# Kernel tuning notes

Measured on AMD Instinct MI355X. Metric: run time of the kernel, lower is better.

## Reference

```python
import jax, jax.numpy as jnp
import numpy as np

NUM_HIGH = 3
CHANNELS = 3

def _gauss_kernel(channels):
    k = jnp.array([[1., 4., 6., 4., 1.],
                   [4., 16., 24., 16., 4.],
                   [6., 24., 36., 24., 6.],
                   [4., 16., 24., 16., 4.],
                   [1., 4., 6., 4., 1.]], dtype=jnp.float32) / 256.0
    # depthwise kernel layout OIHW with I=1, O=channels
    return jnp.broadcast_to(k, (channels, 1, 5, 5))

def conv_gauss(img, kernel):
    # reflect-pad by 2 on H,W then depthwise (grouped) 5x5 conv, VALID
    p = jnp.pad(img, ((0, 0), (0, 0), (2, 2), (2, 2)), mode='reflect')
    return jax.lax.conv_general_dilated(
        p, kernel, window_strides=(1, 1), padding='VALID',
        feature_group_count=img.shape[1],
        dimension_numbers=('NCHW', 'OIHW', 'NCHW'))

def downsample(x):
    return x[:, :, ::2, ::2]

def upsample(x, kernel):
    B, C, H, W = x.shape
    x_up = jnp.zeros((B, C, 2 * H, 2 * W), dtype=x.dtype).at[:, :, ::2, ::2].set(x)
    return conv_gauss(x_up, 4.0 * kernel)

def setup_inputs() -> dict:
    key = jax.random.key(0)
    img = jax.random.normal(key, (8, CHANNELS, 1024, 1024), dtype=jnp.float32)
    kernel = _gauss_kernel(CHANNELS)
    return {"img": img, "kernel": kernel}

def reference(img, kernel):
    # pyramid_decom: Laplacian pyramid (H,W divisible by 2**NUM_HIGH, so no interpolate)
    current = img
    pyr = []
    for _ in range(NUM_HIGH):
        filtered = conv_gauss(current, kernel)
        down = downsample(filtered)
        up = upsample(down, kernel)
        pyr.append(current - up)
        current = down
    pyr.append(current)
    return tuple(pyr)
```

## Files before the change

kernel.cpp:

```cpp
#include <hip/hip_runtime.h>

#define TILE 64
#define SCW 72
#define SCP 76
#define SDW 34
#define SDP 36

__device__ __forceinline__ int refl(int t, int n) {
    if (t < 0) t = -t;
    if (t >= n) t = 2 * (n - 1) - t;
    return t;
}

__global__ __launch_bounds__(256) void lap_level_kernel(
    const float* __restrict__ cur, float* __restrict__ lap,
    float* __restrict__ down, int H, int W)
{
    __shared__ float s_cur[SCW][SCP];
    __shared__ float s_down[SDW][SDP];

    const int x0 = blockIdx.x * TILE, y0 = blockIdx.y * TILE;
    const int img = blockIdx.z;
    const int Hh = H >> 1, Wh = W >> 1;
    const int tid = threadIdx.x;
    const int tx = tid & 15, ty = tid >> 4;

    const float* curb = cur + (size_t)img * H * W;

    const bool border = (x0 == 0) | (y0 == 0) | (x0 + TILE == W) | (y0 + TILE == H);
    if (!border) {
        const float* src = curb + (size_t)(y0 - 4) * W + (x0 - 4);
        for (int k = tid; k < SCW * 18; k += 256) {
            unsigned r = (unsigned)k / 18u;
            unsigned c4 = (unsigned)k - r * 18u;
            *(float4*)&s_cur[r][c4 * 4] =
                *(const float4*)(src + (size_t)r * W + c4 * 4);
        }
    } else {
        for (int k = tid; k < SCW * SCW; k += 256) {
            unsigned r = (unsigned)k / 72u;
            unsigned c = (unsigned)k - r * 72u;
            s_cur[r][c] = curb[(size_t)refl(y0 - 4 + (int)r, H) * W
                               + refl(x0 - 4 + (int)c, W)];
        }
    }
    __syncthreads();

    const int dy0 = (y0 >> 1) - 1, dx0 = (x0 >> 1) - 1;
    float* downb = down + (size_t)img * Hh * Wh;
    for (int k = tid; k < SDW * SDW; k += 256) {
        unsigned dy = (unsigned)k / 34u;
        unsigned dx = (unsigned)k - dy * 34u;
        const int rb = 2 * (int)dy, cb = 2 * (int)dx;
        float acc = 0.f;
        const float wr[5] = {1.f, 4.f, 6.f, 4.f, 1.f};
#pragma unroll
        for (int u = 0; u < 5; ++u) {
            const float* row = &s_cur[rb + u][cb];
            float2 p0 = *(const float2*)(row);
            float2 p1 = *(const float2*)(row + 2);
            float2 p2 = *(const float2*)(row + 4);
            float rs = p0.x + 4.f * p0.y + 6.f * p1.x + 4.f * p1.y + p2.x;
            acc += wr[u] * rs;
        }
        acc *= (1.0f / 256.0f);
        s_down[dy][dx] = acc;
        if (dy - 1u < 32u && dx - 1u < 32u)
            downb[(size_t)(dy0 + (int)dy) * Wh + (dx0 + (int)dx)] = acc;
    }
    __syncthreads();

    float d[4][4];
#pragma unroll
    for (int r = 0; r < 4; ++r) {
        float2 a = *(const float2*)&s_down[2 * ty + r][2 * tx];
        float2 b = *(const float2*)&s_down[2 * ty + r][2 * tx + 2];
        d[r][0] = a.x; d[r][1] = a.y; d[r][2] = b.x; d[r][3] = b.y;
    }
    float ve[2][4], vo[2][4];
#pragma unroll
    for (int r2 = 0; r2 < 2; ++r2)
#pragma unroll
        for (int c = 0; c < 4; ++c) {
            ve[r2][c] = d[r2][c] + 6.f * d[r2 + 1][c] + d[r2 + 2][c];
            vo[r2][c] = 4.f * (d[r2 + 1][c] + d[r2 + 2][c]);
        }

    float* lapb = lap + (size_t)img * H * W;
    const int ib = y0 + 4 * ty, jb = x0 + 4 * tx;
#pragma unroll
    for (int rr = 0; rr < 4; ++rr) {
        const int r2 = rr >> 1;
        float4 cv = *(const float4*)&s_cur[4 * ty + 4 + rr][4 * tx + 4];
        float u0, u1, u2, u3;
        if ((rr & 1) == 0) {
            u0 = ve[r2][0] + 6.f * ve[r2][1] + ve[r2][2];
            u1 = 4.f * (ve[r2][1] + ve[r2][2]);
            u2 = ve[r2][1] + 6.f * ve[r2][2] + ve[r2][3];
            u3 = 4.f * (ve[r2][2] + ve[r2][3]);
        } else {
            u0 = vo[r2][0] + 6.f * vo[r2][1] + vo[r2][2];
            u1 = 4.f * (vo[r2][1] + vo[r2][2]);
            u2 = vo[r2][1] + 6.f * vo[r2][2] + vo[r2][3];
            u3 = 4.f * (vo[r2][2] + vo[r2][3]);
        }
        float4 o;
        o.x = cv.x - u0 * (1.f / 64.f);
        o.y = cv.y - u1 * (1.f / 64.f);
        o.z = cv.z - u2 * (1.f / 64.f);
        o.w = cv.w - u3 * (1.f / 64.f);
        *(float4*)(lapb + (size_t)(ib + rr) * W + jb) = o;
    }
}

extern "C" void kernel_launch(void* const* d_in, const int* in_sizes, int n_in,
                              void* d_out, int out_size, void* d_ws, size_t ws_size,
                              hipStream_t stream) {
    const float* img = (const float*)d_in[0];
    float* out = (float*)d_out;

    const long long BC = 8LL * 3;
    const long long n0 = BC * 1024 * 1024;
    const long long n1 = BC * 512 * 512;
    const long long n2 = BC * 256 * 256;

    float* out0 = out;
    float* out1 = out0 + n0;
    float* out2 = out1 + n1;
    float* out3 = out2 + n2;

    float* ws0 = (float*)d_ws;
    float* ws1 = ws0 + n1;

    lap_level_kernel<<<dim3(1024 / TILE, 1024 / TILE, (int)BC), 256, 0, stream>>>(
        img, out0, ws0, 1024, 1024);
    lap_level_kernel<<<dim3(512 / TILE, 512 / TILE, (int)BC), 256, 0, stream>>>(
        ws0, out1, ws1, 512, 512);
    lap_level_kernel<<<dim3(256 / TILE, 256 / TILE, (int)BC), 256, 0, stream>>>(
        ws1, out2, out3, 256, 256);
}
```

Before: 86.77 us.

## Fuse first two pyramid levels into one kernel with enlarged halo tile

Adds a kernel that computes levels 0 and 1 in a single pass. Each block loads an 83x83 halo tile, builds the level-1 downsample and the level-2 downsample in shared memory, and writes both Laplacian outputs plus the quarter-resolution image. This removes one launch and the global write and reread of the level-1 intermediate. In exchange it recomputes overlapping halos, uses more shared memory per block, and needs reflect-index handling at the second level.

```diff
diff --git a/kernel.cpp b/kernel.cpp
--- a/kernel.cpp
+++ b/kernel.cpp
@@ -1,16 +1,183 @@
 #include <hip/hip_runtime.h>
 
 #define TILE 64
-#define SCW 72
-#define SCP 76
-#define SDW 34
-#define SDP 36
 
 __device__ __forceinline__ int refl(int t, int n) {
     if (t < 0) t = -t;
     if (t >= n) t = 2 * (n - 1) - t;
     return t;
 }
+
+#define SC_H 83
+#define SC_W 84
+#define D0_N 39
+#define D0_P 40
+#define D1_N 18
+#define D1_P 20
+
+__global__ __launch_bounds__(256) void lap2level_kernel(
+    const float* __restrict__ cur, float* __restrict__ lap0,
+    float* __restrict__ lap1, float* __restrict__ down1,
+    int H, int W)
+{
+    __shared__ float s_cur[SC_H][SC_W];
+    __shared__ float s_d0[D0_N][D0_P];
+    __shared__ float s_d1[D1_N][D1_P];
+
+    const int x0 = blockIdx.x * TILE, y0 = blockIdx.y * TILE;
+    const int img = blockIdx.z;
+    const int Hh = H >> 1, Wh = W >> 1, Wq = W >> 2;
+    const int tid = threadIdx.x;
+    const int tx = tid & 15, ty = tid >> 4;
+
+    const float* curb = cur + (size_t)img * H * W;
+
+    const bool border = (x0 == 0) | (y0 == 0) | (x0 + TILE == W) | (y0 + TILE == H);
+    if (!border) {
+        const float* src = curb + (size_t)(y0 - 12) * W + (x0 - 12);
+        for (int k = tid; k < SC_H * 21; k += 256) {
+            unsigned r = (unsigned)k / 21u;
+            unsigned c4 = (unsigned)k - r * 21u;
+            *(float4*)&s_cur[r][c4 * 4] = *(const float4*)(src + (size_t)r * W + c4 * 4);
+        }
+    } else {
+        for (int k = tid; k < SC_H * SC_H; k += 256) {
+            unsigned r = (unsigned)k / 83u;
+            unsigned c = (unsigned)k - r * 83u;
+            s_cur[r][c] = curb[(size_t)refl(y0 - 12 + (int)r, H) * W
+                               + refl(x0 - 12 + (int)c, W)];
+        }
+    }
+    __syncthreads();
+
+    for (int k = tid; k < D0_N * D0_N; k += 256) {
+        unsigned a = (unsigned)k / 39u;
+        unsigned b = (unsigned)k - a * 39u;
+        const int rb = 2 * (int)a + 2, cb = 2 * (int)b + 2;
+        const float wv[5] = {1.f, 4.f, 6.f, 4.f, 1.f};
+        float acc = 0.f;
+#pragma unroll
+        for (int u = 0; u < 5; ++u) {
+            const float* row = &s_cur[rb + u][cb];
+            float2 p0 = *(const float2*)row;
+            float2 p1 = *(const float2*)(row + 2);
+            float rs = p0.x + 4.f * p0.y + 6.f * p1.x + 4.f * p1.y + row[4];
+            acc += wv[u] * rs;
+        }
+        s_d0[a][b] = acc * (1.0f / 256.0f);
+    }
+    __syncthreads();
+
+    const int dy0f = (y0 >> 1) - 4, dx0f = (x0 >> 1) - 4;
+    for (int k = tid; k < D1_N * D1_N; k += 256) {
+        unsigned e = (unsigned)k / 18u;
+        unsigned f = (unsigned)k - e * 18u;
+        int ar[5], bc[5];
+#pragma unroll
+        for (int u = 0; u < 5; ++u) {
+            int dyt = dy0f + 2 * (int)e + u;
+            int ov = dyt - (Hh - 1); if (ov < 0) ov = 0;
+            ar[u] = 2 * (int)e + u - 2 * ov;
+            int dxt = dx0f + 2 * (int)f + u;
+            int ow = dxt - (Wh - 1); if (ow < 0) ow = 0;
+            bc[u] = 2 * (int)f + u - 2 * ow;
+        }
+        const float wv[5] = {1.f, 4.f, 6.f, 4.f, 1.f};
+        float acc = 0.f;
+#pragma unroll
+        for (int u = 0; u < 5; ++u) {
+            float rs = 0.f;
+#pragma unroll
+            for (int v = 0; v < 5; ++v) rs += wv[v] * s_d0[ar[u]][bc[v]];
+            acc += wv[u] * rs;
+        }
+        s_d1[e][f] = acc * (1.0f / 256.0f);
+    }
+    __syncthreads();
+
+    {
+        float* d1b = down1 + (size_t)img * (Hh >> 1) * Wq;
+        int e = (tid >> 4) + 1, f = (tid & 15) + 1;
+        d1b[(size_t)((y0 >> 2) + e - 1) * Wq + ((x0 >> 2) + f - 1)] = s_d1[e][f];
+    }
+
+    {
+        float d[4][4];
+#pragma unroll
+        for (int r = 0; r < 4; ++r)
+#pragma unroll
+            for (int c = 0; c < 4; ++c)
+                d[r][c] = s_d0[2 * ty + 3 + r][2 * tx + 3 + c];
+        float ve[2][4], vo[2][4];
+#pragma unroll
+        for (int r2 = 0; r2 < 2; ++r2)
+#pragma unroll
+            for (int c = 0; c < 4; ++c) {
+                ve[r2][c] = d[r2][c] + 6.f * d[r2 + 1][c] + d[r2 + 2][c];
+                vo[r2][c] = 4.f * (d[r2 + 1][c] + d[r2 + 2][c]);
+            }
+        float* lap0b = lap0 + (size_t)img * H * W;
+        const int ib = y0 + 4 * ty, jb = x0 + 4 * tx;
+#pragma unroll
+        for (int rr = 0; rr < 4; ++rr) {
+            const int r2 = rr >> 1;
+            float4 cv = *(const float4*)&s_cur[4 * ty + 12 + rr][4 * tx + 12];
+            float u0, u1, u2, u3;
+            if ((rr & 1) == 0) {
+                u0 = ve[r2][0] + 6.f * ve[r2][1] + ve[r2][2];
+                u1 = 4.f * (ve[r2][1] + ve[r2][2]);
+                u2 = ve[r2][1] + 6.f * ve[r2][2] + ve[r2][3];
+                u3 = 4.f * (ve[r2][2] + ve[r2][3]);
+            } else {
+                u0 = vo[r2][0] + 6.f * vo[r2][1] + vo[r2][2];
+                u1 = 4.f * (vo[r2][1] + vo[r2][2]);
+                u2 = vo[r2][1] + 6.f * vo[r2][2] + vo[r2][3];
+                u3 = 4.f * (vo[r2][2] + vo[r2][3]);
+            }
+            float4 o;
+            o.x = cv.x - u0 * (1.f / 64.f);
+            o.y = cv.y - u1 * (1.f / 64.f);
+            o.z = cv.z - u2 * (1.f / 64.f);
+            o.w = cv.w - u3 * (1.f / 64.f);
+            *(float4*)(lap0b + (size_t)(ib + rr) * W + jb) = o;
+        }
+    }
+
+    {
+        float m[3][3];
+#pragma unroll
+        for (int a = 0; a < 3; ++a)
+#pragma unroll
+            for (int b = 0; b < 3; ++b)
+                m[a][b] = s_d1[ty + a][tx + b];
+        float ce[3], co[3];
+#pragma unroll
+        for (int c = 0; c < 3; ++c) {
+            ce[c] = m[0][c] + 6.f * m[1][c] + m[2][c];
+            co[c] = 4.f * (m[1][c] + m[2][c]);
+        }
+        float u00 = ce[0] + 6.f * ce[1] + ce[2];
+        float u01 = 4.f * (ce[1] + ce[2]);
+        float u10 = co[0] + 6.f * co[1] + co[2];
+        float u11 = 4.f * (co[1] + co[2]);
+        float2 c0 = *(const float2*)&s_d0[2 * ty + 4][2 * tx + 4];
+        float2 c1 = *(const float2*)&s_d0[2 * ty + 5][2 * tx + 4];
+        float* lap1b = lap1 + (size_t)img * Hh * Wh;
+        const int p0 = (y0 >> 1) + 2 * ty, q0 = (x0 >> 1) + 2 * tx;
+        float2 o0, o1;
+        o0.x = c0.x - u00 * (1.f / 64.f);
+        o0.y = c0.y - u01 * (1.f / 64.f);
+        o1.x = c1.x - u10 * (1.f / 64.f);
+        o1.y = c1.y - u11 * (1.f / 64.f);
+        *(float2*)(lap1b + (size_t)p0 * Wh + q0) = o0;
+        *(float2*)(lap1b + (size_t)(p0 + 1) * Wh + q0) = o1;
+    }
+}
+
+#define SCW 72
+#define SCP 76
+#define SDW 34
+#define SDP 36
 
 __global__ __launch_bounds__(256) void lap_level_kernel(
     const float* __restrict__ cur, float* __restrict__ lap,
@@ -33,8 +200,7 @@
         for (int k = tid; k < SCW * 18; k += 256) {
             unsigned r = (unsigned)k / 18u;
             unsigned c4 = (unsigned)k - r * 18u;
-            *(float4*)&s_cur[r][c4 * 4] =
-                *(const float4*)(src + (size_t)r * W + c4 * 4);
+            *(float4*)&s_cur[r][c4 * 4] = *(const float4*)(src + (size_t)r * W + c4 * 4);
         }
     } else {
         for (int k = tid; k < SCW * SCW; k += 256) {
@@ -52,16 +218,15 @@
         unsigned dy = (unsigned)k / 34u;
         unsigned dx = (unsigned)k - dy * 34u;
         const int rb = 2 * (int)dy, cb = 2 * (int)dx;
+        const float wv[5] = {1.f, 4.f, 6.f, 4.f, 1.f};
         float acc = 0.f;
-        const float wr[5] = {1.f, 4.f, 6.f, 4.f, 1.f};
 #pragma unroll
         for (int u = 0; u < 5; ++u) {
             const float* row = &s_cur[rb + u][cb];
             float2 p0 = *(const float2*)(row);
             float2 p1 = *(const float2*)(row + 2);
-            float2 p2 = *(const float2*)(row + 4);
-            float rs = p0.x + 4.f * p0.y + 6.f * p1.x + 4.f * p1.y + p2.x;
-            acc += wr[u] * rs;
+            float rs = p0.x + 4.f * p0.y + 6.f * p1.x + 4.f * p1.y + row[4];
+            acc += wv[u] * rs;
         }
         acc *= (1.0f / 256.0f);
         s_down[dy][dx] = acc;
@@ -130,12 +295,9 @@
     float* out3 = out2 + n2;
 
     float* ws0 = (float*)d_ws;
-    float* ws1 = ws0 + n1;
-
-    lap_level_kernel<<<dim3(1024 / TILE, 1024 / TILE, (int)BC), 256, 0, stream>>>(
-        img, out0, ws0, 1024, 1024);
-    lap_level_kernel<<<dim3(512 / TILE, 512 / TILE, (int)BC), 256, 0, stream>>>(
-        ws0, out1, ws1, 512, 512);
+
+    lap2level_kernel<<<dim3(16, 16, (int)BC), 256, 0, stream>>>(
+        img, out0, out1, ws0, 1024, 1024);
     lap_level_kernel<<<dim3(256 / TILE, 256 / TILE, (int)BC), 256, 0, stream>>>(
-        ws1, out2, out3, 256, 256);
+        ws0, out2, out3, 256, 256);
 }
```

After: 86.48 us. Within noise of the previous version (-0.3%).

## Separate the downsample blur into vertical and horizontal passes, use 512-thread blocks

Applied to the files above, without the earlier changes.

The 5x5 blur that produces the downsampled tile is split into a vertical pass, which writes into a new shared scratch buffer, and a horizontal pass that reads from it. This cuts the multiply-adds per output. The block grows to 512 threads, so each thread now produces two output rows instead of four, and the launch bound requests 8 blocks per CU. The cost is an extra barrier, about 10 KB more shared memory per block, and padding changes that may alter bank-conflict behaviour.

```diff
diff --git a/kernel.cpp b/kernel.cpp
--- a/kernel.cpp
+++ b/kernel.cpp
@@ -1,10 +1,9 @@
 #include <hip/hip_runtime.h>
 
 #define TILE 64
-#define SCW 72
 #define SCP 76
-#define SDW 34
-#define SDP 36
+#define TMP 77
+#define SDP 35
 
 __device__ __forceinline__ int refl(int t, int n) {
     if (t < 0) t = -t;
@@ -12,32 +11,31 @@
     return t;
 }
 
-__global__ __launch_bounds__(256) void lap_level_kernel(
+__global__ __launch_bounds__(512, 8) void lap_level_kernel(
     const float* __restrict__ cur, float* __restrict__ lap,
     float* __restrict__ down, int H, int W)
 {
-    __shared__ float s_cur[SCW][SCP];
-    __shared__ float s_down[SDW][SDP];
+    __shared__ float s_cur[72][SCP];
+    __shared__ float s_tmp[34][TMP];
+    __shared__ float s_down[34][SDP];
 
     const int x0 = blockIdx.x * TILE, y0 = blockIdx.y * TILE;
     const int img = blockIdx.z;
     const int Hh = H >> 1, Wh = W >> 1;
     const int tid = threadIdx.x;
-    const int tx = tid & 15, ty = tid >> 4;
 
     const float* curb = cur + (size_t)img * H * W;
 
     const bool border = (x0 == 0) | (y0 == 0) | (x0 + TILE == W) | (y0 + TILE == H);
     if (!border) {
         const float* src = curb + (size_t)(y0 - 4) * W + (x0 - 4);
-        for (int k = tid; k < SCW * 18; k += 256) {
+        for (int k = tid; k < 72 * 18; k += 512) {
             unsigned r = (unsigned)k / 18u;
-            unsigned c4 = (unsigned)k - r * 18u;
-            *(float4*)&s_cur[r][c4 * 4] =
-                *(const float4*)(src + (size_t)r * W + c4 * 4);
+            unsigned c4 = ((unsigned)k - r * 18u) * 4u;
+            *(float4*)&s_cur[r][c4] = *(const float4*)(src + (size_t)r * W + c4);
         }
     } else {
-        for (int k = tid; k < SCW * SCW; k += 256) {
+        for (int k = tid; k < 72 * 72; k += 512) {
             unsigned r = (unsigned)k / 72u;
             unsigned c = (unsigned)k - r * 72u;
             s_cur[r][c] = curb[(size_t)refl(y0 - 4 + (int)r, H) * W
@@ -46,71 +44,63 @@
     }
     __syncthreads();
 
-    const int dy0 = (y0 >> 1) - 1, dx0 = (x0 >> 1) - 1;
-    float* downb = down + (size_t)img * Hh * Wh;
-    for (int k = tid; k < SDW * SDW; k += 256) {
-        unsigned dy = (unsigned)k / 34u;
-        unsigned dx = (unsigned)k - dy * 34u;
-        const int rb = 2 * (int)dy, cb = 2 * (int)dx;
-        float acc = 0.f;
-        const float wr[5] = {1.f, 4.f, 6.f, 4.f, 1.f};
-#pragma unroll
-        for (int u = 0; u < 5; ++u) {
-            const float* row = &s_cur[rb + u][cb];
-            float2 p0 = *(const float2*)(row);
-            float2 p1 = *(const float2*)(row + 2);
-            float2 p2 = *(const float2*)(row + 4);
-            float rs = p0.x + 4.f * p0.y + 6.f * p1.x + 4.f * p1.y + p2.x;
-            acc += wr[u] * rs;
-        }
-        acc *= (1.0f / 256.0f);
-        s_down[dy][dx] = acc;
-        if (dy - 1u < 32u && dx - 1u < 32u)
-            downb[(size_t)(dy0 + (int)dy) * Wh + (dx0 + (int)dx)] = acc;
+    for (int k = tid; k < 34 * 18; k += 512) {
+        unsigned a = (unsigned)k / 18u;
+        unsigned c4 = ((unsigned)k - a * 18u) * 4u;
+        float4 r0 = *(const float4*)&s_cur[2 * a + 0][c4];
+        float4 r1 = *(const float4*)&s_cur[2 * a + 1][c4];
+        float4 r2 = *(const float4*)&s_cur[2 * a + 2][c4];
+        float4 r3 = *(const float4*)&s_cur[2 * a + 3][c4];
+        float4 r4 = *(const float4*)&s_cur[2 * a + 4][c4];
+        s_tmp[a][c4 + 0] = r0.x + 4.f * r1.x + 6.f * r2.x + 4.f * r3.x + r4.x;
+        s_tmp[a][c4 + 1] = r0.y + 4.f * r1.y + 6.f * r2.y + 4.f * r3.y + r4.y;
+        s_tmp[a][c4 + 2] = r0.z + 4.f * r1.z + 6.f * r2.z + 4.f * r3.z + r4.z;
+        s_tmp[a][c4 + 3] = r0.w + 4.f * r1.w + 6.f * r2.w + 4.f * r3.w + r4.w;
     }
     __syncthreads();
 
-    float d[4][4];
+    float* downb = down + (size_t)img * Hh * Wh;
+    for (int k = tid; k < 34 * 34; k += 512) {
+        unsigned a = (unsigned)k / 34u;
+        unsigned b = (unsigned)k - a * 34u;
+        const float* t = &s_tmp[a][2 * b];
+        float v = (t[0] + 4.f * t[1] + 6.f * t[2] + 4.f * t[3] + t[4]) * (1.f / 256.f);
+        s_down[a][b] = v;
+        if (a - 1u < 32u && b - 1u < 32u)
+            downb[(size_t)((y0 >> 1) + (int)a - 1) * Wh + ((x0 >> 1) + (int)b - 1)] = v;
+    }
+    __syncthreads();
+
+    const int tx = tid & 15, ty = tid >> 4;
+    float d0[4], d1[4], d2[4];
 #pragma unroll
-    for (int r = 0; r < 4; ++r) {
-        float2 a = *(const float2*)&s_down[2 * ty + r][2 * tx];
-        float2 b = *(const float2*)&s_down[2 * ty + r][2 * tx + 2];
-        d[r][0] = a.x; d[r][1] = a.y; d[r][2] = b.x; d[r][3] = b.y;
+    for (int c = 0; c < 4; ++c) {
+        d0[c] = s_down[ty + 0][2 * tx + c];
+        d1[c] = s_down[ty + 1][2 * tx + c];
+        d2[c] = s_down[ty + 2][2 * tx + c];
     }
-    float ve[2][4], vo[2][4];
+    float ce[4], co[4];
 #pragma unroll
-    for (int r2 = 0; r2 < 2; ++r2)
-#pragma unroll
-        for (int c = 0; c < 4; ++c) {
-            ve[r2][c] = d[r2][c] + 6.f * d[r2 + 1][c] + d[r2 + 2][c];
-            vo[r2][c] = 4.f * (d[r2 + 1][c] + d[r2 + 2][c]);
-        }
+    for (int c = 0; c < 4; ++c) {
+        ce[c] = d0[c] + 6.f * d1[c] + d2[c];
+        co[c] = 4.f * (d1[c] + d2[c]);
+    }
+    float4 cve = *(const float4*)&s_cur[4 + 2 * ty][4 + 4 * tx];
+    float4 cvo = *(const float4*)&s_cur[5 + 2 * ty][4 + 4 * tx];
+    float4 oe, oo;
+    oe.x = cve.x - (ce[0] + 6.f * ce[1] + ce[2]) * (1.f / 64.f);
+    oe.y = cve.y - 4.f * (ce[1] + ce[2]) * (1.f / 64.f);
+    oe.z = cve.z - (ce[1] + 6.f * ce[2] + ce[3]) * (1.f / 64.f);
+    oe.w = cve.w - 4.f * (ce[2] + ce[3]) * (1.f / 64.f);
+    oo.x = cvo.x - (co[0] + 6.f * co[1] + co[2]) * (1.f / 64.f);
+    oo.y = cvo.y - 4.f * (co[1] + co[2]) * (1.f / 64.f);
+    oo.z = cvo.z - (co[1] + 6.f * co[2] + co[3]) * (1.f / 64.f);
+    oo.w = cvo.w - 4.f * (co[2] + co[3]) * (1.f / 64.f);
 
     float* lapb = lap + (size_t)img * H * W;
-    const int ib = y0 + 4 * ty, jb = x0 + 4 * tx;
-#pragma unroll
-    for (int rr = 0; rr < 4; ++rr) {
-        const int r2 = rr >> 1;
-        float4 cv = *(const float4*)&s_cur[4 * ty + 4 + rr][4 * tx + 4];
-        float u0, u1, u2, u3;
-        if ((rr & 1) == 0) {
-            u0 = ve[r2][0] + 6.f * ve[r2][1] + ve[r2][2];
-            u1 = 4.f * (ve[r2][1] + ve[r2][2]);
-            u2 = ve[r2][1] + 6.f * ve[r2][2] + ve[r2][3];
-            u3 = 4.f * (ve[r2][2] + ve[r2][3]);
-        } else {
-            u0 = vo[r2][0] + 6.f * vo[r2][1] + vo[r2][2];
-            u1 = 4.f * (vo[r2][1] + vo[r2][2]);
-            u2 = vo[r2][1] + 6.f * vo[r2][2] + vo[r2][3];
-            u3 = 4.f * (vo[r2][2] + vo[r2][3]);
-        }
-        float4 o;
-        o.x = cv.x - u0 * (1.f / 64.f);
-        o.y = cv.y - u1 * (1.f / 64.f);
-        o.z = cv.z - u2 * (1.f / 64.f);
-        o.w = cv.w - u3 * (1.f / 64.f);
-        *(float4*)(lapb + (size_t)(ib + rr) * W + jb) = o;
-    }
+    const int i0 = y0 + 2 * ty, j0 = x0 + 4 * tx;
+    *(float4*)(lapb + (size_t)i0 * W + j0) = oe;
+    *(float4*)(lapb + (size_t)(i0 + 1) * W + j0) = oo;
 }
 
 extern "C" void kernel_launch(void* const* d_in, const int* in_sizes, int n_in,
@@ -132,10 +122,10 @@
     float* ws0 = (float*)d_ws;
     float* ws1 = ws0 + n1;
 
-    lap_level_kernel<<<dim3(1024 / TILE, 1024 / TILE, (int)BC), 256, 0, stream>>>(
+    lap_level_kernel<<<dim3(1024 / TILE, 1024 / TILE, (int)BC), 512, 0, stream>>>(
         img, out0, ws0, 1024, 1024);
-    lap_level_kernel<<<dim3(512 / TILE, 512 / TILE, (int)BC), 256, 0, stream>>>(
+    lap_level_kernel<<<dim3(512 / TILE, 512 / TILE, (int)BC), 512, 0, stream>>>(
         ws0, out1, ws1, 512, 512);
-    lap_level_kernel<<<dim3(256 / TILE, 256 / TILE, (int)BC), 256, 0, stream>>>(
+    lap_level_kernel<<<dim3(256 / TILE, 256 / TILE, (int)BC), 512, 0, stream>>>(
         ws1, out2, out3, 256, 256);
 }
```

Measured after the change: 84.48 us. 2.6% less time.

## Apply separable vertical blur during global load and shrink shared tile

Applied to the files above, without the earlier changes.

The 72x72 shared input tile is replaced by a 34x72 buffer holding vertically filtered rows, computed at stride 2 directly from global float4 loads with two loads in flight per thread. The horizontal pass then reads this smaller buffer to produce the downsampled values. The center pixels for the Laplacian subtraction are now re-read from global memory instead of shared memory. This cuts LDS footprint and FLOPs and allows a launch_bounds occupancy hint of 6, at the cost of a second global read of the center tile that should mostly hit in cache.

```diff
diff --git a/kernel.cpp b/kernel.cpp
--- a/kernel.cpp
+++ b/kernel.cpp
@@ -1,10 +1,12 @@
 #include <hip/hip_runtime.h>
 
 #define TILE 64
-#define SCW 72
-#define SCP 76
-#define SDW 34
-#define SDP 36
+#define DR 34
+#define NCH 18
+#define TMPP 76
+#define SDP 35
+#define NBV (DR * NCH)
+#define NBH (DR * 17)
 
 __device__ __forceinline__ int refl(int t, int n) {
     if (t < 0) t = -t;
@@ -12,71 +14,97 @@
     return t;
 }
 
-__global__ __launch_bounds__(256) void lap_level_kernel(
+__global__ __launch_bounds__(256, 6) void lap_level_kernel(
     const float* __restrict__ cur, float* __restrict__ lap,
     float* __restrict__ down, int H, int W)
 {
-    __shared__ float s_cur[SCW][SCP];
-    __shared__ float s_down[SDW][SDP];
+    __shared__ float s_tmp[DR][TMPP];
+    __shared__ float s_down[DR][SDP];
 
     const int x0 = blockIdx.x * TILE, y0 = blockIdx.y * TILE;
     const int img = blockIdx.z;
     const int Hh = H >> 1, Wh = W >> 1;
     const int tid = threadIdx.x;
-    const int tx = tid & 15, ty = tid >> 4;
 
     const float* curb = cur + (size_t)img * H * W;
 
     const bool border = (x0 == 0) | (y0 == 0) | (x0 + TILE == W) | (y0 + TILE == H);
     if (!border) {
-        const float* src = curb + (size_t)(y0 - 4) * W + (x0 - 4);
-        for (int k = tid; k < SCW * 18; k += 256) {
-            unsigned r = (unsigned)k / 18u;
-            unsigned c4 = (unsigned)k - r * 18u;
-            *(float4*)&s_cur[r][c4 * 4] =
-                *(const float4*)(src + (size_t)r * W + c4 * 4);
+        for (int k = tid; k < NBV; k += 512) {
+            int a0 = k / NCH, c0 = (k - a0 * NCH) * 4;
+            const float* p0 = curb + (size_t)(y0 - 4 + 2 * a0) * W + (x0 - 4 + c0);
+            float4 A0 = *(const float4*)(p0);
+            float4 A1 = *(const float4*)(p0 + (size_t)W);
+            float4 A2 = *(const float4*)(p0 + (size_t)2 * W);
+            float4 A3 = *(const float4*)(p0 + (size_t)3 * W);
+            float4 A4 = *(const float4*)(p0 + (size_t)4 * W);
+            const int k1 = k + 256;
+            const bool h1 = k1 < NBV;
+            int a1 = 0, c1 = 0;
+            float4 B0, B1, B2, B3, B4;
+            if (h1) {
+                a1 = k1 / NCH; c1 = (k1 - a1 * NCH) * 4;
+                const float* p1 = curb + (size_t)(y0 - 4 + 2 * a1) * W + (x0 - 4 + c1);
+                B0 = *(const float4*)(p1);
+                B1 = *(const float4*)(p1 + (size_t)W);
+                B2 = *(const float4*)(p1 + (size_t)2 * W);
+                B3 = *(const float4*)(p1 + (size_t)3 * W);
+                B4 = *(const float4*)(p1 + (size_t)4 * W);
+            }
+            float4 t0;
+            t0.x = A0.x + 4.f * A1.x + 6.f * A2.x + 4.f * A3.x + A4.x;
+            t0.y = A0.y + 4.f * A1.y + 6.f * A2.y + 4.f * A3.y + A4.y;
+            t0.z = A0.z + 4.f * A1.z + 6.f * A2.z + 4.f * A3.z + A4.z;
+            t0.w = A0.w + 4.f * A1.w + 6.f * A2.w + 4.f * A3.w + A4.w;
+            *(float4*)&s_tmp[a0][c0] = t0;
+            if (h1) {
+                float4 t1;
+                t1.x = B0.x + 4.f * B1.x + 6.f * B2.x + 4.f * B3.x + B4.x;
+                t1.y = B0.y + 4.f * B1.y + 6.f * B2.y + 4.f * B3.y + B4.y;
+                t1.z = B0.z + 4.f * B1.z + 6.f * B2.z + 4.f * B3.z + B4.z;
+                t1.w = B0.w + 4.f * B1.w + 6.f * B2.w + 4.f * B3.w + B4.w;
+                *(float4*)&s_tmp[a1][c1] = t1;
+            }
         }
     } else {
-        for (int k = tid; k < SCW * SCW; k += 256) {
-            unsigned r = (unsigned)k / 72u;
-            unsigned c = (unsigned)k - r * 72u;
-            s_cur[r][c] = curb[(size_t)refl(y0 - 4 + (int)r, H) * W
-                               + refl(x0 - 4 + (int)c, W)];
+        for (int k = tid; k < DR * 72; k += 256) {
+            int a = k / 72, c = k - a * 72;
+            int gx = refl(x0 - 4 + c, W);
+            int r0 = y0 - 4 + 2 * a;
+            const float wv[5] = {1.f, 4.f, 6.f, 4.f, 1.f};
+            float acc = 0.f;
+#pragma unroll
+            for (int u = 0; u < 5; ++u)
+                acc += wv[u] * curb[(size_t)refl(r0 + u, H) * W + gx];
+            s_tmp[a][c] = acc;
         }
     }
     __syncthreads();
 
-    const int dy0 = (y0 >> 1) - 1, dx0 = (x0 >> 1) - 1;
     float* downb = down + (size_t)img * Hh * Wh;
-    for (int k = tid; k < SDW * SDW; k += 256) {
-        unsigned dy = (unsigned)k / 34u;
-        unsigned dx = (unsigned)k - dy * 34u;
-        const int rb = 2 * (int)dy, cb = 2 * (int)dx;
-        float acc = 0.f;
-        const float wr[5] = {1.f, 4.f, 6.f, 4.f, 1.f};
-#pragma unroll
-        for (int u = 0; u < 5; ++u) {
-            const float* row = &s_cur[rb + u][cb];
-            float2 p0 = *(const float2*)(row);
-            float2 p1 = *(const float2*)(row + 2);
-            float2 p2 = *(const float2*)(row + 4);
-            float rs = p0.x + 4.f * p0.y + 6.f * p1.x + 4.f * p1.y + p2.x;
-            acc += wr[u] * rs;
+    for (int k = tid; k < NBH; k += 256) {
+        int a = k / 17, b2 = k - a * 17;
+        float4 A = *(const float4*)&s_tmp[a][4 * b2];
+        float4 B = *(const float4*)&s_tmp[a][4 * b2 + 4];
+        float v0 = (A.x + 4.f * A.y + 6.f * A.z + 4.f * A.w + B.x) * (1.f / 256.f);
+        float v1 = (A.z + 4.f * A.w + 6.f * B.x + 4.f * B.y + B.z) * (1.f / 256.f);
+        s_down[a][2 * b2] = v0;
+        s_down[a][2 * b2 + 1] = v1;
+        if ((unsigned)(a - 1) < 32u) {
+            size_t rowoff = (size_t)((y0 >> 1) - 1 + a) * Wh + ((x0 >> 1) - 1);
+            if (b2 >= 1) downb[rowoff + 2 * b2] = v0;
+            if (b2 <= 15) downb[rowoff + 2 * b2 + 1] = v1;
         }
-        acc *= (1.0f / 256.0f);
-        s_down[dy][dx] = acc;
-        if (dy - 1u < 32u && dx - 1u < 32u)
-            downb[(size_t)(dy0 + (int)dy) * Wh + (dx0 + (int)dx)] = acc;
     }
     __syncthreads();
 
+    const int tx = tid & 15, ty = tid >> 4;
     float d[4][4];
 #pragma unroll
-    for (int r = 0; r < 4; ++r) {
-        float2 a = *(const float2*)&s_down[2 * ty + r][2 * tx];
-        float2 b = *(const float2*)&s_down[2 * ty + r][2 * tx + 2];
-        d[r][0] = a.x; d[r][1] = a.y; d[r][2] = b.x; d[r][3] = b.y;
-    }
+    for (int r = 0; r < 4; ++r)
+#pragma unroll
+        for (int c = 0; c < 4; ++c)
+            d[r][c] = s_down[2 * ty + r][2 * tx + c];
     float ve[2][4], vo[2][4];
 #pragma unroll
     for (int r2 = 0; r2 < 2; ++r2)
@@ -85,13 +113,12 @@
             ve[r2][c] = d[r2][c] + 6.f * d[r2 + 1][c] + d[r2 + 2][c];
             vo[r2][c] = 4.f * (d[r2 + 1][c] + d[r2 + 2][c]);
         }
-
     float* lapb = lap + (size_t)img * H * W;
     const int ib = y0 + 4 * ty, jb = x0 + 4 * tx;
 #pragma unroll
     for (int rr = 0; rr < 4; ++rr) {
         const int r2 = rr >> 1;
-        float4 cv = *(const float4*)&s_cur[4 * ty + 4 + rr][4 * tx + 4];
+        float4 cv = *(const float4*)(curb + (size_t)(ib + rr) * W + jb);
         float u0, u1, u2, u3;
         if ((rr & 1) == 0) {
             u0 = ve[r2][0] + 6.f * ve[r2][1] + ve[r2][2];
```

New measurement: 92.88 us. 1.07x slower.
